# Kernel tuning notes

Hardware: AMD Instinct MI355X
Metric: run time of the kernel (lower is better)

Reference implementation:

```python
import jax, jax.numpy as jnp
import numpy as np

B, NLAT, NLON = 32, 721, 1440


def setup_inputs() -> dict:
    key = jax.random.key(0)
    k1, k2 = jax.random.split(key)
    lsm = jax.random.randint(k1, (B, NLAT, NLON), 0, 2).astype(jnp.int32)  # 0=ocean, 1=land
    vals = jax.random.normal(k2, (B, NLAT, NLON), dtype=jnp.float32)
    sst = jnp.where(lsm == 0, vals, jnp.nan)  # NaN over land, like real SST fields
    return {"sst": sst, "lsm": lsm}


def _circular_fill(sst, lsm):
    # Vectorized equivalent of the per-row masked circular linear interpolation.
    # On a uniform periodic lon grid, lon distances are proportional to circular
    # index distances, so interp1d over the tripled-longitude ocean points reduces
    # to: for each lon j, find previous/next ocean index (circularly) and lerp.
    L = sst.shape[-1]
    f32 = sst.dtype
    m = (lsm == 0) & ~jnp.isnan(sst)                       # ocean mask [B,H,L]
    ar = jnp.arange(L, dtype=jnp.int32)

    # previous ocean index <= j (circular wrap via last ocean point - L)
    a_prev = jnp.where(m, ar, -1)
    prev = jax.lax.cummax(a_prev, axis=2)
    last = prev[..., -1:]
    prev = jnp.where(prev < 0, last - L, prev)

    # next ocean index >= j (circular wrap via first ocean point + L)
    a_next = jnp.where(m, ar, 2 * L)
    nxt = jax.lax.cummin(a_next, axis=2, reverse=True)
    first = nxt[..., :1]
    nxt = jnp.where(nxt >= 2 * L, first + L, nxt)

    sst_prev = jnp.take_along_axis(sst, prev % L, axis=2)
    sst_next = jnp.take_along_axis(sst, nxt % L, axis=2)

    dtot = nxt - prev                                       # >= 0; 0 exactly at ocean points
    dp = ar - prev                                          # >= 0
    t = jnp.where(dtot > 0,
                  dp.astype(f32) / jnp.maximum(dtot, 1).astype(f32),
                  jnp.zeros((), f32))
    v = sst_prev * (1.0 - t) + sst_next * t                 # single-ocean-point rows -> constant
    row_valid = m.any(axis=2, keepdims=True)
    v = jnp.where(row_valid, v, jnp.nan)                    # no ocean points -> NaN row

    # Fill all latitude rows after the last valid row with that row's values
    H = sst.shape[1]
    hidx = jnp.arange(H, dtype=jnp.int32)
    lastrow = jnp.max(jnp.where(row_valid[..., 0], hidx[None, :], -1), axis=1)  # [B]
    bidx = jnp.arange(sst.shape[0])
    fill = v[bidx, jnp.clip(lastrow, 0)]                    # [B, L]
    cond = (hidx[None, :, None] > lastrow[:, None, None]) & (lastrow[:, None, None] >= 0)
    v = jnp.where(cond, fill[:, None, :], v)

    # Restore original SST wherever it was valid (ocean_mask = ~isnan(sst))
    return jnp.where(jnp.isnan(sst), v, sst)


def reference(sst, lsm):
    return _circular_fill(sst, lsm)
```

## Files before the change

kernel.cpp:

```cpp
#include <hip/hip_runtime.h>
#include <cstdint>

#define LON 1440
#define LAT 721
#define NB  32
#define NW32 45
#define NV   360
#define BS   384

typedef float f32x4 __attribute__((ext_vector_type(4)));

__device__ __forceinline__ bool is_nan_f(float v) {
    return (__float_as_uint(v) & 0x7fffffffu) > 0x7f800000u;
}

__global__ __launch_bounds__(BS) void fill_rows(const float4* __restrict__ sst4,
                                                float4*       __restrict__ out4,
                                                unsigned char* __restrict__ rowflag) {
    __shared__ float s[LON];
    __shared__ unsigned int msk[NW32 + 3];

    const int r = blockIdx.x;
    const size_t base4 = (size_t)r * NV;
    const int tid = threadIdx.x;

    float4 sv = make_float4(0.f, 0.f, 0.f, 0.f);
    unsigned nib = 0u;
    if (tid < NV) {
        sv = sst4[base4 + tid];
        ((float4*)s)[tid] = sv;
        nib = (!is_nan_f(sv.x) ? 1u : 0u) | (!is_nan_f(sv.y) ? 2u : 0u)
            | (!is_nan_f(sv.z) ? 4u : 0u) | (!is_nan_f(sv.w) ? 8u : 0u);
    }
    unsigned part = nib << (4 * (tid & 7));
    part |= __shfl_xor(part, 1);
    part |= __shfl_xor(part, 2);
    part |= __shfl_xor(part, 4);
    if ((tid & 7) == 0 && tid < NV) msk[tid >> 3] = part;
    __syncthreads();

    int first = -1, last = -1;
    for (int w = 0; w < NW32; ++w) {
        unsigned mw = msk[w];
        if (mw) { first = w * 32 + (__ffs(mw) - 1); break; }
    }
    if (first >= 0) {
        for (int w = NW32 - 1; w >= 0; --w) {
            unsigned mw = msk[w];
            if (mw) { last = w * 32 + (31 - __clz(mw)); break; }
        }
    }
    if (tid == 0) rowflag[r] = (first >= 0) ? 1 : 0;

    if (tid < NV) {
        float res[4] = {sv.x, sv.y, sv.z, sv.w};
        if (first >= 0 && nib != 0xFu) {
            const int w = tid >> 3;
            const unsigned mw = msk[w];
            #pragma unroll
            for (int j = 0; j < 4; ++j) {
                if (!(nib & (1u << j))) {
                    const int i = 4 * tid + j;
                    const int bpos = i & 31;
                    unsigned bits = mw & (0xffffffffu >> (31 - bpos));
                    int ww = w;
                    while (bits == 0u && ww > 0) bits = msk[--ww];
                    int prev = bits ? (ww * 32 + (31 - __clz(bits)))
                                    : (last - LON);
                    bits = mw & (0xffffffffu << bpos);
                    ww = w;
                    while (bits == 0u && ww < NW32 - 1) bits = msk[++ww];
                    int nxt = bits ? (ww * 32 + (__ffs(bits) - 1))
                                   : (first + LON);
                    float t  = (float)(i - prev)
                             * __builtin_amdgcn_rcpf((float)(nxt - prev));
                    float sp = s[prev < 0    ? prev + LON : prev];
                    float sn = s[nxt  >= LON ? nxt  - LON : nxt];
                    res[j] = fmaf(t, sn - sp, sp);
                }
            }
        }
        f32x4 rv;
        rv.x = res[0]; rv.y = res[1]; rv.z = res[2]; rv.w = res[3];
        __builtin_nontemporal_store(rv, (f32x4*)&out4[base4 + tid]);
    }
}

__global__ __launch_bounds__(256) void fill_tail(const float* __restrict__ sst,
                                                 float*       __restrict__ out,
                                                 const unsigned char* __restrict__ rowflag) {
    const int b = blockIdx.x;
    const int tid = threadIdx.x;
    __shared__ int red[256];
    int lr = -1;
    for (int h = tid; h < LAT; h += 256)
        if (rowflag[b * LAT + h]) lr = h;
    red[tid] = lr;
    __syncthreads();
    for (int off = 128; off > 0; off >>= 1) {
        if (tid < off) red[tid] = max(red[tid], red[tid + off]);
        __syncthreads();
    }
    lr = red[0];
    if (lr < 0 || lr == LAT - 1) return;
    const size_t fb = ((size_t)b * LAT + lr) * LON;
    for (int h = lr + 1; h < LAT; ++h) {
        const size_t base = ((size_t)b * LAT + h) * LON;
        for (int i = tid; i < LON; i += 256) {
            float svv = sst[base + i];
            out[base + i] = is_nan_f(svv) ? out[fb + i] : svv;
        }
    }
}

extern "C" void kernel_launch(void* const* d_in, const int* in_sizes, int n_in,
                              void* d_out, int out_size, void* d_ws, size_t ws_size,
                              hipStream_t stream) {
    const float4* sst4 = (const float4*)d_in[0];
    float4* out4 = (float4*)d_out;
    unsigned char* rowflag = (unsigned char*)d_ws;

    fill_rows<<<NB * LAT, BS, 0, stream>>>(sst4, out4, rowflag);
    fill_tail<<<NB, 256, 0, stream>>>((const float*)d_in[0], (float*)d_out, rowflag);
}
```

Measured before the change: 287.5 us.

## Process one row per wavefront, removing block barriers and shared row staging

Each 64-lane wavefront now handles a whole latitude row, with four rows per 256-thread block. Every lane loads six float4 chunks into registers. The per-row mask lives in per-wave shared memory and needs only an LDS waitcnt instead of __syncthreads. The row values are no longer staged in shared memory, so neighbour values for interpolation are gathered straight from global memory (mostly L1/L2 hits). The aim is to cut block-level synchronisation and shared-memory traffic and to raise occupancy, at the cost of more registers and scattered global reads for land points.

```diff
diff --git a/kernel.cpp b/kernel.cpp
--- a/kernel.cpp
+++ b/kernel.cpp
@@ -6,7 +6,8 @@
 #define NB  32
 #define NW32 45
 #define NV   360
-#define BS   384
+#define RPB 4
+#define BS  (RPB * 64)
 
 typedef float f32x4 __attribute__((ext_vector_type(4)));
 
@@ -14,75 +15,97 @@
     return (__float_as_uint(v) & 0x7fffffffu) > 0x7f800000u;
 }
 
-__global__ __launch_bounds__(BS) void fill_rows(const float4* __restrict__ sst4,
-                                                float4*       __restrict__ out4,
-                                                unsigned char* __restrict__ rowflag) {
-    __shared__ float s[LON];
-    __shared__ unsigned int msk[NW32 + 3];
+__device__ __forceinline__ unsigned pack_nib(f32x4 v) {
+    return (!is_nan_f(v.x) ? 1u : 0u) | (!is_nan_f(v.y) ? 2u : 0u)
+         | (!is_nan_f(v.z) ? 4u : 0u) | (!is_nan_f(v.w) ? 8u : 0u);
+}
 
-    const int r = blockIdx.x;
-    const size_t base4 = (size_t)r * NV;
-    const int tid = threadIdx.x;
+__global__ __launch_bounds__(BS, 8) void fill_rows(const f32x4* __restrict__ sst4,
+                                                   const float* __restrict__ sst,
+                                                   f32x4*       __restrict__ out4,
+                                                   unsigned char* __restrict__ rowflag) {
+    __shared__ unsigned int msk[RPB][48];
 
-    float4 sv = make_float4(0.f, 0.f, 0.f, 0.f);
-    unsigned nib = 0u;
-    if (tid < NV) {
-        sv = sst4[base4 + tid];
-        ((float4*)s)[tid] = sv;
-        nib = (!is_nan_f(sv.x) ? 1u : 0u) | (!is_nan_f(sv.y) ? 2u : 0u)
-            | (!is_nan_f(sv.z) ? 4u : 0u) | (!is_nan_f(sv.w) ? 8u : 0u);
+    const int tid  = threadIdx.x;
+    const int lane = tid & 63;
+    const int wv   = tid >> 6;
+    const int r    = blockIdx.x * RPB + wv;
+    const size_t base4   = (size_t)r * NV;
+    const size_t rowbase = (size_t)r * LON;
+
+    f32x4 sv[6];
+    unsigned nib[6];
+    #pragma unroll
+    for (int k = 0; k < 6; ++k) {
+        const int c = 64 * k + lane;
+        if (c < NV) {
+            sv[k] = sst4[base4 + c];
+            nib[k] = pack_nib(sv[k]);
+        } else {
+            sv[k] = (f32x4){0.f, 0.f, 0.f, 0.f};
+            nib[k] = 0u;
+        }
     }
-    unsigned part = nib << (4 * (tid & 7));
-    part |= __shfl_xor(part, 1);
-    part |= __shfl_xor(part, 2);
-    part |= __shfl_xor(part, 4);
-    if ((tid & 7) == 0 && tid < NV) msk[tid >> 3] = part;
-    __syncthreads();
+
+    #pragma unroll
+    for (int k = 0; k < 6; ++k) {
+        unsigned part = nib[k] << (4 * (lane & 7));
+        part |= __shfl_xor(part, 1);
+        part |= __shfl_xor(part, 2);
+        part |= __shfl_xor(part, 4);
+        const int w = 8 * k + (lane >> 3);
+        if ((lane & 7) == 0 && w < NW32) msk[wv][w] = part;
+    }
+    asm volatile("s_waitcnt lgkmcnt(0)" ::: "memory");
 
     int first = -1, last = -1;
     for (int w = 0; w < NW32; ++w) {
-        unsigned mw = msk[w];
+        unsigned mw = msk[wv][w];
         if (mw) { first = w * 32 + (__ffs(mw) - 1); break; }
     }
     if (first >= 0) {
         for (int w = NW32 - 1; w >= 0; --w) {
-            unsigned mw = msk[w];
+            unsigned mw = msk[wv][w];
             if (mw) { last = w * 32 + (31 - __clz(mw)); break; }
         }
     }
-    if (tid == 0) rowflag[r] = (first >= 0) ? 1 : 0;
+    if (lane == 0) rowflag[r] = (first >= 0) ? 1 : 0;
 
-    if (tid < NV) {
-        float res[4] = {sv.x, sv.y, sv.z, sv.w};
-        if (first >= 0 && nib != 0xFu) {
-            const int w = tid >> 3;
-            const unsigned mw = msk[w];
+    #pragma unroll
+    for (int k = 0; k < 6; ++k) {
+        const int c = 64 * k + lane;
+        if (c >= NV) continue;
+        f32x4 rv = sv[k];
+        const unsigned nb = nib[k];
+        if (first >= 0 && nb != 0xFu) {
+            const int w = c >> 3;
+            const unsigned mw = msk[wv][w];
+            float res[4] = {rv.x, rv.y, rv.z, rv.w};
             #pragma unroll
             for (int j = 0; j < 4; ++j) {
-                if (!(nib & (1u << j))) {
-                    const int i = 4 * tid + j;
+                if (!(nb & (1u << j))) {
+                    const int i = 4 * c + j;
                     const int bpos = i & 31;
                     unsigned bits = mw & (0xffffffffu >> (31 - bpos));
                     int ww = w;
-                    while (bits == 0u && ww > 0) bits = msk[--ww];
+                    while (bits == 0u && ww > 0) bits = msk[wv][--ww];
                     int prev = bits ? (ww * 32 + (31 - __clz(bits)))
                                     : (last - LON);
                     bits = mw & (0xffffffffu << bpos);
                     ww = w;
-                    while (bits == 0u && ww < NW32 - 1) bits = msk[++ww];
+                    while (bits == 0u && ww < NW32 - 1) bits = msk[wv][++ww];
                     int nxt = bits ? (ww * 32 + (__ffs(bits) - 1))
                                    : (first + LON);
                     float t  = (float)(i - prev)
                              * __builtin_amdgcn_rcpf((float)(nxt - prev));
-                    float sp = s[prev < 0    ? prev + LON : prev];
-                    float sn = s[nxt  >= LON ? nxt  - LON : nxt];
+                    float sp = sst[rowbase + (prev < 0    ? prev + LON : prev)];
+                    float sn = sst[rowbase + (nxt  >= LON ? nxt  - LON : nxt)];
                     res[j] = fmaf(t, sn - sp, sp);
                 }
             }
+            rv.x = res[0]; rv.y = res[1]; rv.z = res[2]; rv.w = res[3];
         }
-        f32x4 rv;
-        rv.x = res[0]; rv.y = res[1]; rv.z = res[2]; rv.w = res[3];
-        __builtin_nontemporal_store(rv, (f32x4*)&out4[base4 + tid]);
+        __builtin_nontemporal_store(rv, (f32x4*)&out4[base4 + c]);
     }
 }
 
@@ -116,10 +139,11 @@
 extern "C" void kernel_launch(void* const* d_in, const int* in_sizes, int n_in,
                               void* d_out, int out_size, void* d_ws, size_t ws_size,
                               hipStream_t stream) {
-    const float4* sst4 = (const float4*)d_in[0];
-    float4* out4 = (float4*)d_out;
+    const f32x4* sst4 = (const f32x4*)d_in[0];
+    f32x4* out4 = (f32x4*)d_out;
     unsigned char* rowflag = (unsigned char*)d_ws;
 
-    fill_rows<<<NB * LAT, BS, 0, stream>>>(sst4, out4, rowflag);
+    fill_rows<<<(NB * LAT) / RPB, BS, 0, stream>>>(sst4, (const float*)d_in[0],
+                                                   out4, rowflag);
     fill_tail<<<NB, 256, 0, stream>>>((const float*)d_in[0], (float*)d_out, rowflag);
 }
```

Measured after the change: 304.6 us. 5.9% more time.
